# Optimization experiments

Measured on AMD Instinct MI355X. Metric: run time of the kernel, lower is better.

The kernel has to match this reference:

```python
import jax, jax.numpy as jnp
import numpy as np

D2 = 200  # 2*D with D=100, hidden size of H and U

def setup_inputs() -> dict:
    key = jax.random.key(0)
    k1, k2, k3, k4 = jax.random.split(key, 4)
    B, T, J = 64, 2048, 128
    H = jax.random.normal(k1, (B, T, D2), dtype=jnp.float32)
    U = jax.random.normal(k2, (B, J, D2), dtype=jnp.float32)
    # alpha = nn.Linear(6D, 1): weight [600], bias scalar
    bound = 1.0 / np.sqrt(6 * 100)
    w = jax.random.uniform(k3, (3 * D2,), minval=-bound, maxval=bound, dtype=jnp.float32)
    b = jax.random.uniform(k4, (), minval=-bound, maxval=bound, dtype=jnp.float32)
    return {"H": H, "U": U, "w": w, "b": b}

def reference(H, U, w, b):
    # Trilinear similarity S[b,t,j] = alpha([H_t; U_j; H_t*U_j]) decomposed:
    # identical math to concat+linear, without materializing [B,T*J,6D].
    w_h, w_u, w_m = w[:D2], w[D2:2 * D2], w[2 * D2:]
    S = (jnp.einsum('btd,d->bt', H, w_h)[:, :, None]
         + jnp.einsum('bjd,d->bj', U, w_u)[:, None, :]
         + jnp.einsum('btd,d,bjd->btj', H, w_m, U)
         + b)  # [B,T,J]
    C2Q_att = jax.nn.softmax(S, axis=-1)            # [B,T,J]
    U_tilde = jnp.einsum('btj,bjd->btd', C2Q_att, U)  # [B,T,2D]
    Q2C_att = jax.nn.softmax(jnp.max(S, axis=-1), axis=-1)  # [B,T]
    H_tilde = jnp.einsum('bt,btd->bd', Q2C_att, H)[:, None, :]  # [B,1,2D]
    T = H.shape[1]
    H_tilde_rep = jnp.broadcast_to(H_tilde, H.shape)  # repeat(1,T,1)
    G = jnp.concatenate([H, U_tilde, H * U_tilde, H * H_tilde_rep], axis=-1)  # [B,T,8D]
    return G, Q2C_att[:, None, :]
```

## Files before the change

### kernel.cpp

```cpp
#include <hip/hip_runtime.h>
#include <math.h>

typedef __attribute__((ext_vector_type(8))) short bf16x8;
typedef __attribute__((ext_vector_type(4))) float f32x4;

#define Bb 64
#define Tt 2048
#define Jj 128
#define Dd 200
#define GD 800
#define TILE 64
#define NTH 1024

#define OFF_USH 0u
#define OFF_UJT 57344u
#define OFF_HMS 110592u
#define OFF_PSH 139264u
#define OFF_SUS 155648u
#define OFF_SHS 156160u
#define OFF_SMX 156416u
#define OFF_SSM 157440u
#define SMEM_BYTES 158464u

__device__ __forceinline__ unsigned short f2bf(float f) {
    union { float f; unsigned u; } v; v.f = f;
    unsigned r = v.u + 0x7FFFu + ((v.u >> 16) & 1u);
    return (unsigned short)(r >> 16);
}

__device__ __forceinline__ bf16x8 pack8(f32x4 a, f32x4 b) {
    bf16x8 o;
    o[0] = (short)f2bf(a[0]); o[1] = (short)f2bf(a[1]);
    o[2] = (short)f2bf(a[2]); o[3] = (short)f2bf(a[3]);
    o[4] = (short)f2bf(b[0]); o[5] = (short)f2bf(b[1]);
    o[6] = (short)f2bf(b[2]); o[7] = (short)f2bf(b[3]);
    return o;
}

__global__ __launch_bounds__(NTH) void k_main(
    const float* __restrict__ H, const float* __restrict__ U,
    const float* __restrict__ wt, const float* __restrict__ bptr,
    float* __restrict__ G, float* __restrict__ mrow)
{
    __shared__ __align__(16) char smem[SMEM_BYTES];

    const int tid  = threadIdx.x;
    const int lane = tid & 63;
    const int wv   = tid >> 6;

    const int lin = blockIdx.x;
    const int wg  = (lin & 7) * 256 + (lin >> 3);
    const int b   = wg >> 5;
    const int t0  = (wg & 31) * TILE;

    const float* Hb = H + ((size_t)b * Tt + t0) * Dd;
    const float* Ub = U + (size_t)b * Jj * Dd;
    const float  bb = bptr[0];

    const float wh0 = wt[lane], wh1 = wt[64 + lane], wh2 = wt[128 + lane];
    const float wh3 = (lane < 8) ? wt[192 + lane] : 0.f;
    const float wu0 = wt[200 + lane], wu1 = wt[264 + lane], wu2 = wt[328 + lane];
    const float wu3 = (lane < 8) ? wt[392 + lane] : 0.f;

    for (int i = tid; i < 128 * 28; i += NTH) {
        int row = i / 28, c8 = i % 28;
        bf16x8 val = {0,0,0,0,0,0,0,0};
        if (c8 < 25) {
            const float* p = Ub + row * Dd + c8 * 8;
            val = pack8(*(const f32x4*)p, *(const f32x4*)(p + 4));
        }
        unsigned a = OFF_USH + (unsigned)row * 448u + (unsigned)c8 * 16u;
        *(bf16x8*)(smem + (a ^ ((unsigned)(row & 7) << 4))) = val;
    }
    for (int i = tid; i < TILE * 28; i += NTH) {
        int row = i / 28, c8 = i % 28;
        bf16x8 val = {0,0,0,0,0,0,0,0};
        if (c8 < 25) {
            const float* p  = Hb + row * Dd + c8 * 8;
            const float* wp = wt + 400 + c8 * 8;
            f32x4 h0 = *(const f32x4*)p,        h1 = *(const f32x4*)(p + 4);
            f32x4 w0 = *(const f32x4*)wp,       w1 = *(const f32x4*)(wp + 4);
            val = pack8(h0 * w0, h1 * w1);
        }
        unsigned a = OFF_HMS + (unsigned)row * 448u + (unsigned)c8 * 16u;
        *(bf16x8*)(smem + (a ^ ((unsigned)(row & 7) << 4))) = val;
    }
    for (int jj = 0; jj < 8; ++jj) {
        int j = wv * 8 + jj;
        const float* up = Ub + j * Dd;
        float v = up[lane] * wu0 + up[64 + lane] * wu1 + up[128 + lane] * wu2;
        if (lane < 8) v += up[192 + lane] * wu3;
        #pragma unroll
        for (int off = 32; off; off >>= 1) v += __shfl_xor(v, off);
        if (lane == 0) *(float*)(smem + OFF_SUS + (unsigned)j * 4u) = v + bb;
    }
    for (int rr = 0; rr < 4; ++rr) {
        int row = wv * 4 + rr;
        const float* hp = Hb + row * Dd;
        float v = hp[lane] * wh0 + hp[64 + lane] * wh1 + hp[128 + lane] * wh2;
        if (lane < 8) v += hp[192 + lane] * wh3;
        #pragma unroll
        for (int off = 32; off; off >>= 1) v += __shfl_xor(v, off);
        if (lane == 0) *(float*)(smem + OFF_SHS + (unsigned)row * 4u) = v;
    }
    __syncthreads();

    for (int i = tid; i < 208 * 64; i += NTH) {
        int d  = i >> 6;
        int jp = (i & 63) << 1;
        unsigned short v0 = 0, v1 = 0;
        if (d < Dd) {
            unsigned a0 = OFF_USH + (unsigned)jp * 448u + ((unsigned)d << 1);
            v0 = *(const unsigned short*)(smem + (a0 ^ ((unsigned)(jp & 7) << 4)));
            unsigned a1 = OFF_USH + (unsigned)(jp + 1) * 448u + ((unsigned)d << 1);
            v1 = *(const unsigned short*)(smem + (a1 ^ ((unsigned)((jp + 1) & 7) << 4)));
        }
        unsigned pk = (unsigned)v0 | ((unsigned)v1 << 16);
        unsigned wa = OFF_UJT + (unsigned)d * 256u + (unsigned)((i & 63) << 2);
        *(unsigned*)(smem + (wa ^ ((unsigned)(d & 7) << 4))) = pk;
    }

    const int rg = wv >> 2, cgS = wv & 3;
    const int rowA = rg * 16 + (lane & 15);
    const unsigned kfo = (unsigned)(((lane >> 4) << 4));
    f32x4 accS0 = {0.f, 0.f, 0.f, 0.f}, accS1 = {0.f, 0.f, 0.f, 0.f};
    #pragma unroll
    for (int ki = 0; ki < 7; ++ki) {
        unsigned ab = OFF_HMS + (unsigned)rowA * 448u + (unsigned)ki * 64u + kfo;
        bf16x8 af = *(const bf16x8*)(smem + (ab ^ ((unsigned)(rowA & 7) << 4)));
        int j0 = cgS * 32 + (lane & 15);
        unsigned b0 = OFF_USH + (unsigned)j0 * 448u + (unsigned)ki * 64u + kfo;
        bf16x8 bf0 = *(const bf16x8*)(smem + (b0 ^ ((unsigned)(j0 & 7) << 4)));
        accS0 = __builtin_amdgcn_mfma_f32_16x16x32_bf16(af, bf0, accS0, 0, 0, 0);
        int j1 = j0 + 16;
        unsigned b1 = OFF_USH + (unsigned)j1 * 448u + (unsigned)ki * 64u + kfo;
        bf16x8 bf1 = *(const bf16x8*)(smem + (b1 ^ ((unsigned)(j1 & 7) << 4)));
        accS1 = __builtin_amdgcn_mfma_f32_16x16x32_bf16(af, bf1, accS1, 0, 0, 0);
    }
    __syncthreads();

    const int rowBase = rg * 16 + ((lane >> 4) << 2);
    const float su0 = *(const float*)(smem + OFF_SUS + (unsigned)(cgS * 32 + (lane & 15)) * 4u);
    const float su1 = *(const float*)(smem + OFF_SUS + (unsigned)(cgS * 32 + 16 + (lane & 15)) * 4u);
    f32x4 sh4 = *(const f32x4*)(smem + OFF_SHS + (unsigned)rowBase * 4u);
    float s0a[4], s1a[4], e0a[4], e1a[4];
    #pragma unroll
    for (int r = 0; r < 4; ++r) {
        float s0 = accS0[r] + sh4[r] + su0;
        float s1 = accS1[r] + sh4[r] + su1;
        s0a[r] = s0; s1a[r] = s1;
        float m = fmaxf(s0, s1);
        m = fmaxf(m, __shfl_xor(m, 1));
        m = fmaxf(m, __shfl_xor(m, 2));
        m = fmaxf(m, __shfl_xor(m, 4));
        m = fmaxf(m, __shfl_xor(m, 8));
        if ((lane & 15) == 0)
            *(float*)(smem + OFF_SMX + (unsigned)((rowBase + r) * 4 + cgS) * 4u) = m;
    }
    __syncthreads();
    #pragma unroll
    for (int r = 0; r < 4; ++r) {
        f32x4 mx4 = *(const f32x4*)(smem + OFF_SMX + (unsigned)(rowBase + r) * 16u);
        float M = fmaxf(fmaxf(mx4[0], mx4[1]), fmaxf(mx4[2], mx4[3]));
        float e0 = __expf(s0a[r] - M), e1 = __expf(s1a[r] - M);
        e0a[r] = e0; e1a[r] = e1;
        float s = e0 + e1;
        s += __shfl_xor(s, 1); s += __shfl_xor(s, 2);
        s += __shfl_xor(s, 4); s += __shfl_xor(s, 8);
        if ((lane & 15) == 0)
            *(float*)(smem + OFF_SSM + (unsigned)((rowBase + r) * 4 + cgS) * 4u) = s;
        if (cgS == 0 && (lane & 15) == 0)
            mrow[(size_t)b * Tt + t0 + rowBase + r] = M;
    }
    __syncthreads();
    #pragma unroll
    for (int r = 0; r < 4; ++r) {
        f32x4 sm4 = *(const f32x4*)(smem + OFF_SSM + (unsigned)(rowBase + r) * 16u);
        float inv = 1.f / (sm4[0] + sm4[1] + sm4[2] + sm4[3]);
        float p0 = e0a[r] * inv, p1 = e1a[r] * inv;
        float pn0 = __shfl_down(p0, 1), pn1 = __shfl_down(p1, 1);
        if (!(lane & 1)) {
            int row = rowBase + r;
            int col0 = cgS * 32 + (lane & 15);
            unsigned swz = (unsigned)(row & 7) << 4;
            unsigned a0 = OFF_PSH + (unsigned)row * 256u + (unsigned)col0 * 2u;
            *(unsigned*)(smem + (a0 ^ swz)) = (unsigned)f2bf(p0) | ((unsigned)f2bf(pn0) << 16);
            unsigned a1 = a0 + 32u;
            *(unsigned*)(smem + (a1 ^ swz)) = (unsigned)f2bf(p1) | ((unsigned)f2bf(pn1) << 16);
        }
    }
    __syncthreads();

    const int rg2 = wv >> 2, cg2 = wv & 3;
    const int start = (cg2 == 0) ? 0 : (3 * cg2 + 1);
    const int cnt   = (cg2 == 0) ? 4 : 3;
    const int rowA2 = rg2 * 16 + (lane & 15);
    f32x4 accP0 = {0.f,0.f,0.f,0.f}, accP1 = {0.f,0.f,0.f,0.f};
    f32x4 accP2 = {0.f,0.f,0.f,0.f}, accP3 = {0.f,0.f,0.f,0.f};
    #pragma unroll
    for (int ki = 0; ki < 4; ++ki) {
        unsigned ab = OFF_PSH + (unsigned)rowA2 * 256u + (unsigned)ki * 64u + kfo;
        bf16x8 af = *(const bf16x8*)(smem + (ab ^ ((unsigned)(rowA2 & 7) << 4)));
        int d0 = start * 16 + (lane & 15);
        {
            unsigned bb0 = OFF_UJT + (unsigned)d0 * 256u + (unsigned)ki * 64u + kfo;
            bf16x8 bf = *(const bf16x8*)(smem + (bb0 ^ ((unsigned)(d0 & 7) << 4)));
            accP0 = __builtin_amdgcn_mfma_f32_16x16x32_bf16(af, bf, accP0, 0, 0, 0);
        }
        {
            int d = d0 + 16;
            unsigned bb1 = OFF_UJT + (unsigned)d * 256u + (unsigned)ki * 64u + kfo;
            bf16x8 bf = *(const bf16x8*)(smem + (bb1 ^ ((unsigned)(d & 7) << 4)));
            accP1 = __builtin_amdgcn_mfma_f32_16x16x32_bf16(af, bf, accP1, 0, 0, 0);
        }
        {
            int d = d0 + 32;
            unsigned bb2 = OFF_UJT + (unsigned)d * 256u + (unsigned)ki * 64u + kfo;
            bf16x8 bf = *(const bf16x8*)(smem + (bb2 ^ ((unsigned)(d & 7) << 4)));
            accP2 = __builtin_amdgcn_mfma_f32_16x16x32_bf16(af, bf, accP2, 0, 0, 0);
        }
        if (cnt == 4) {
            int d = d0 + 48;
            unsigned bb3 = OFF_UJT + (unsigned)d * 256u + (unsigned)ki * 64u + kfo;
            bf16x8 bf = *(const bf16x8*)(smem + (bb3 ^ ((unsigned)(d & 7) << 4)));
            accP3 = __builtin_amdgcn_mfma_f32_16x16x32_bf16(af, bf, accP3, 0, 0, 0);
        }
    }
    __syncthreads();

    {
        const int rowW = rg2 * 16 + ((lane >> 4) << 2);
        const int c0 = start * 16 + (lane & 15);
        #pragma unroll
        for (int r = 0; r < 4; ++r) {
            int row = rowW + r;
            float* base = (float*)(smem + OFF_UJT + (unsigned)row * 816u);
            base[c0]      = accP0[r];
            base[c0 + 16] = accP1[r];
            if (c0 + 32 < Dd) base[c0 + 32] = accP2[r];
            if (cnt == 4)     base[c0 + 48] = accP3[r];
        }
    }
    __syncthreads();

    for (int i = tid; i < TILE * 50; i += NTH) {
        int row = i / 50, c = i % 50;
        f32x4 ut = *(const f32x4*)(smem + OFF_UJT + (unsigned)row * 816u + (unsigned)c * 16u);
        f32x4 h4 = *(const f32x4*)(Hb + row * Dd + c * 4);
        float* grow = G + ((size_t)b * Tt + t0 + row) * GD + c * 4;
        *(f32x4*)(grow)       = h4;
        *(f32x4*)(grow + 200) = ut;
        *(f32x4*)(grow + 400) = h4 * ut;
    }
}

__global__ __launch_bounds__(256) void k_q(
    const float* __restrict__ mrow, float* __restrict__ q)
{
    __shared__ float red[4];
    __shared__ float sM, sS;
    const int b = blockIdx.x, tid = threadIdx.x;
    const int lane = tid & 63, wv = tid >> 6;
    const float* mb = mrow + (size_t)b * Tt;

    float lm = -1e30f;
    for (int i = tid; i < Tt; i += 256) lm = fmaxf(lm, mb[i]);
    #pragma unroll
    for (int off = 32; off; off >>= 1) lm = fmaxf(lm, __shfl_xor(lm, off));
    if (lane == 0) red[wv] = lm;
    __syncthreads();
    if (tid == 0) sM = fmaxf(fmaxf(red[0], red[1]), fmaxf(red[2], red[3]));
    __syncthreads();
    const float M = sM;

    float ls = 0.f;
    for (int i = tid; i < Tt; i += 256) ls += __expf(mb[i] - M);
    #pragma unroll
    for (int off = 32; off; off >>= 1) ls += __shfl_xor(ls, off);
    __syncthreads();
    if (lane == 0) red[wv] = ls;
    __syncthreads();
    if (tid == 0) sS = red[0] + red[1] + red[2] + red[3];
    __syncthreads();
    const float invS = 1.f / sS;

    for (int i = tid; i < Tt; i += 256)
        q[(size_t)b * Tt + i] = __expf(mb[i] - M) * invS;
}

__global__ __launch_bounds__(256) void k_ht(
    const float* __restrict__ H, const float* __restrict__ q,
    float* __restrict__ htil)
{
    const int b = blockIdx.y, ch = blockIdx.x;
    const int d4 = threadIdx.x & 63;
    const int tp = threadIdx.x >> 6;
    if (d4 >= 50) return;
    const float* Hb = H + (size_t)b * Tt * Dd;
    const float* qb = q + (size_t)b * Tt;
    f32x4 acc = {0.f, 0.f, 0.f, 0.f};
    const int tbase = ch * 128 + tp * 32;
    for (int k = 0; k < 32; ++k) {
        int t = tbase + k;
        f32x4 h4 = *(const f32x4*)(Hb + (size_t)t * Dd + d4 * 4);
        acc += h4 * qb[t];
    }
    float* hp = htil + b * Dd + d4 * 4;
    atomicAdd(hp + 0, acc[0]); atomicAdd(hp + 1, acc[1]);
    atomicAdd(hp + 2, acc[2]); atomicAdd(hp + 3, acc[3]);
}

__global__ __launch_bounds__(256) void k_g3(
    const float* __restrict__ H, const float* __restrict__ htil,
    float* __restrict__ G)
{
    const int idx = blockIdx.x * 256 + threadIdx.x;
    if (idx >= Bb * Tt * Dd) return;
    const int d  = idx % Dd;
    const int bt = idx / Dd;
    const int b  = bt >> 11;
    G[(size_t)bt * GD + 600 + d] = H[idx] * htil[b * Dd + d];
}

extern "C" void kernel_launch(void* const* d_in, const int* in_sizes, int n_in,
                              void* d_out, int out_size, void* d_ws, size_t ws_size,
                              hipStream_t stream)
{
    const float* H    = (const float*)d_in[0];
    const float* U    = (const float*)d_in[1];
    const float* wt   = (const float*)d_in[2];
    const float* bptr = (const float*)d_in[3];

    float* G    = (float*)d_out;
    float* q    = G + (size_t)Bb * Tt * GD;
    float* mrow = (float*)d_ws;
    float* htil = mrow + (size_t)Bb * Tt;

    hipMemsetAsync(htil, 0, (size_t)Bb * Dd * sizeof(float), stream);

    k_main<<<(Tt / TILE) * Bb, NTH, 0, stream>>>(H, U, wt, bptr, G, mrow);

    k_q<<<Bb, 256, 0, stream>>>(mrow, q);

    dim3 g2(Tt / 128, Bb);
    k_ht<<<g2, 256, 0, stream>>>(H, q, htil);

    const int n3 = Bb * Tt * Dd;
    k_g3<<<(n3 + 255) / 256, 256, 0, stream>>>(H, htil, G);
}
```

Measured before the change: 712.3 us.

## Make main kernel persistent over 16 tiles with double-buffered H staging

```diff
diff --git a/kernel.cpp b/kernel.cpp
--- a/kernel.cpp
+++ b/kernel.cpp
@@ -9,18 +9,20 @@
 #define Jj 128
 #define Dd 200
 #define GD 800
-#define TILE 64
+#define TILE 32
+#define NT 16
+#define ROWS_BLK (TILE*NT)
 #define NTH 1024
 
 #define OFF_USH 0u
 #define OFF_UJT 57344u
 #define OFF_HMS 110592u
 #define OFF_PSH 139264u
-#define OFF_SUS 155648u
-#define OFF_SHS 156160u
-#define OFF_SMX 156416u
-#define OFF_SSM 157440u
-#define SMEM_BYTES 158464u
+#define OFF_SUS 147456u
+#define OFF_SHS 147968u
+#define OFF_SMX 148224u
+#define OFF_SSM 149248u
+#define SMEM_BYTES 150272u
 
 __device__ __forceinline__ unsigned short f2bf(float f) {
     union { float f; unsigned u; } v; v.f = f;
@@ -37,6 +39,30 @@
     return o;
 }
 
+__device__ __forceinline__ void stage_h(char* smem, const float* __restrict__ Hrows,
+                                        int tid, int buf,
+                                        f32x4 wmA, f32x4 wmB, f32x4 whA, f32x4 whB)
+{
+    const int row = tid >> 5, c = tid & 31;
+    float shp = 0.f;
+    bf16x8 val = {0,0,0,0,0,0,0,0};
+    if (c < 25) {
+        const float* p = Hrows + row * Dd + c * 8;
+        f32x4 h0 = *(const f32x4*)p, h1 = *(const f32x4*)(p + 4);
+        shp = h0[0]*whA[0] + h0[1]*whA[1] + h0[2]*whA[2] + h0[3]*whA[3]
+            + h1[0]*whB[0] + h1[1]*whB[1] + h1[2]*whB[2] + h1[3]*whB[3];
+        val = pack8(h0 * wmA, h1 * wmB);
+    }
+    if (c < 28) {
+        unsigned a = OFF_HMS + (unsigned)buf * 14336u + (unsigned)row * 448u + (unsigned)c * 16u;
+        *(bf16x8*)(smem + (a ^ ((unsigned)(row & 7) << 4))) = val;
+    }
+    #pragma unroll
+    for (int off = 16; off; off >>= 1) shp += __shfl_xor(shp, off);
+    if ((tid & 31) == 0)
+        *(float*)(smem + OFF_SHS + (unsigned)buf * 128u + (unsigned)row * 4u) = shp;
+}
+
 __global__ __launch_bounds__(NTH) void k_main(
     const float* __restrict__ H, const float* __restrict__ U,
     const float* __restrict__ wt, const float* __restrict__ bptr,
@@ -48,17 +74,20 @@
     const int lane = tid & 63;
     const int wv   = tid >> 6;
 
-    const int lin = blockIdx.x;
-    const int wg  = (lin & 7) * 256 + (lin >> 3);
-    const int b   = wg >> 5;
-    const int t0  = (wg & 31) * TILE;
+    const int swz = ((blockIdx.x & 7) << 5) | (blockIdx.x >> 3);
+    const int b   = swz >> 2;
+    const int t0  = (swz & 3) * ROWS_BLK;
 
     const float* Hb = H + ((size_t)b * Tt + t0) * Dd;
     const float* Ub = U + (size_t)b * Jj * Dd;
     const float  bb = bptr[0];
 
-    const float wh0 = wt[lane], wh1 = wt[64 + lane], wh2 = wt[128 + lane];
-    const float wh3 = (lane < 8) ? wt[192 + lane] : 0.f;
+    const int cc = tid & 31;
+    f32x4 whA = {0,0,0,0}, whB = {0,0,0,0}, wmA = {0,0,0,0}, wmB = {0,0,0,0};
+    if (cc < 25) {
+        whA = *(const f32x4*)(wt + cc * 8);       whB = *(const f32x4*)(wt + cc * 8 + 4);
+        wmA = *(const f32x4*)(wt + 400 + cc * 8); wmB = *(const f32x4*)(wt + 400 + cc * 8 + 4);
+    }
     const float wu0 = wt[200 + lane], wu1 = wt[264 + lane], wu2 = wt[328 + lane];
     const float wu3 = (lane < 8) ? wt[392 + lane] : 0.f;
 
@@ -72,19 +101,7 @@
         unsigned a = OFF_USH + (unsigned)row * 448u + (unsigned)c8 * 16u;
         *(bf16x8*)(smem + (a ^ ((unsigned)(row & 7) << 4))) = val;
     }
-    for (int i = tid; i < TILE * 28; i += NTH) {
-        int row = i / 28, c8 = i % 28;
-        bf16x8 val = {0,0,0,0,0,0,0,0};
-        if (c8 < 25) {
-            const float* p  = Hb + row * Dd + c8 * 8;
-            const float* wp = wt + 400 + c8 * 8;
-            f32x4 h0 = *(const f32x4*)p,        h1 = *(const f32x4*)(p + 4);
-            f32x4 w0 = *(const f32x4*)wp,       w1 = *(const f32x4*)(wp + 4);
-            val = pack8(h0 * w0, h1 * w1);
-        }
-        unsigned a = OFF_HMS + (unsigned)row * 448u + (unsigned)c8 * 16u;
-        *(bf16x8*)(smem + (a ^ ((unsigned)(row & 7) << 4))) = val;
-    }
+    stage_h(smem, Hb, tid, 0, wmA, wmB, whA, whB);
     for (int jj = 0; jj < 8; ++jj) {
         int j = wv * 8 + jj;
         const float* up = Ub + j * Dd;
@@ -93,15 +110,6 @@
         #pragma unroll
         for (int off = 32; off; off >>= 1) v += __shfl_xor(v, off);
         if (lane == 0) *(float*)(smem + OFF_SUS + (unsigned)j * 4u) = v + bb;
-    }
-    for (int rr = 0; rr < 4; ++rr) {
-        int row = wv * 4 + rr;
-        const float* hp = Hb + row * Dd;
-        float v = hp[lane] * wh0 + hp[64 + lane] * wh1 + hp[128 + lane] * wh2;
-        if (lane < 8) v += hp[192 + lane] * wh3;
-        #pragma unroll
-        for (int off = 32; off; off >>= 1) v += __shfl_xor(v, off);
-        if (lane == 0) *(float*)(smem + OFF_SHS + (unsigned)row * 4u) = v;
     }
     __syncthreads();
 
@@ -120,137 +128,131 @@
         *(unsigned*)(smem + (wa ^ ((unsigned)(d & 7) << 4))) = pk;
     }
 
-    const int rg = wv >> 2, cgS = wv & 3;
-    const int rowA = rg * 16 + (lane & 15);
-    const unsigned kfo = (unsigned)(((lane >> 4) << 4));
-    f32x4 accS0 = {0.f, 0.f, 0.f, 0.f}, accS1 = {0.f, 0.f, 0.f, 0.f};
-    #pragma unroll
-    for (int ki = 0; ki < 7; ++ki) {
-        unsigned ab = OFF_HMS + (unsigned)rowA * 448u + (unsigned)ki * 64u + kfo;
-        bf16x8 af = *(const bf16x8*)(smem + (ab ^ ((unsigned)(rowA & 7) << 4)));
-        int j0 = cgS * 32 + (lane & 15);
-        unsigned b0 = OFF_USH + (unsigned)j0 * 448u + (unsigned)ki * 64u + kfo;
-        bf16x8 bf0 = *(const bf16x8*)(smem + (b0 ^ ((unsigned)(j0 & 7) << 4)));
-        accS0 = __builtin_amdgcn_mfma_f32_16x16x32_bf16(af, bf0, accS0, 0, 0, 0);
-        int j1 = j0 + 16;
-        unsigned b1 = OFF_USH + (unsigned)j1 * 448u + (unsigned)ki * 64u + kfo;
-        bf16x8 bf1 = *(const bf16x8*)(smem + (b1 ^ ((unsigned)(j1 & 7) << 4)));
-        accS1 = __builtin_amdgcn_mfma_f32_16x16x32_bf16(af, bf1, accS1, 0, 0, 0);
-    }
-    __syncthreads();
-
-    const int rowBase = rg * 16 + ((lane >> 4) << 2);
-    const float su0 = *(const float*)(smem + OFF_SUS + (unsigned)(cgS * 32 + (lane & 15)) * 4u);
-    const float su1 = *(const float*)(smem + OFF_SUS + (unsigned)(cgS * 32 + 16 + (lane & 15)) * 4u);
-    f32x4 sh4 = *(const f32x4*)(smem + OFF_SHS + (unsigned)rowBase * 4u);
-    float s0a[4], s1a[4], e0a[4], e1a[4];
-    #pragma unroll
-    for (int r = 0; r < 4; ++r) {
-        float s0 = accS0[r] + sh4[r] + su0;
-        float s1 = accS1[r] + sh4[r] + su1;
-        s0a[r] = s0; s1a[r] = s1;
-        float m = fmaxf(s0, s1);
-        m = fmaxf(m, __shfl_xor(m, 1));
-        m = fmaxf(m, __shfl_xor(m, 2));
-        m = fmaxf(m, __shfl_xor(m, 4));
-        m = fmaxf(m, __shfl_xor(m, 8));
-        if ((lane & 15) == 0)
-            *(float*)(smem + OFF_SMX + (unsigned)((rowBase + r) * 4 + cgS) * 4u) = m;
-    }
-    __syncthreads();
-    #pragma unroll
-    for (int r = 0; r < 4; ++r) {
-        f32x4 mx4 = *(const f32x4*)(smem + OFF_SMX + (unsigned)(rowBase + r) * 16u);
-        float M = fmaxf(fmaxf(mx4[0], mx4[1]), fmaxf(mx4[2], mx4[3]));
-        float e0 = __expf(s0a[r] - M), e1 = __expf(s1a[r] - M);
-        e0a[r] = e0; e1a[r] = e1;
-        float s = e0 + e1;
-        s += __shfl_xor(s, 1); s += __shfl_xor(s, 2);
-        s += __shfl_xor(s, 4); s += __shfl_xor(s, 8);
-        if ((lane & 15) == 0)
-            *(float*)(smem + OFF_SSM + (unsigned)((rowBase + r) * 4 + cgS) * 4u) = s;
-        if (cgS == 0 && (lane & 15) == 0)
-            mrow[(size_t)b * Tt + t0 + rowBase + r] = M;
-    }
-    __syncthreads();
-    #pragma unroll
-    for (int r = 0; r < 4; ++r) {
-        f32x4 sm4 = *(const f32x4*)(smem + OFF_SSM + (unsigned)(rowBase + r) * 16u);
-        float inv = 1.f / (sm4[0] + sm4[1] + sm4[2] + sm4[3]);
-        float p0 = e0a[r] * inv, p1 = e1a[r] * inv;
-        float pn0 = __shfl_down(p0, 1), pn1 = __shfl_down(p1, 1);
-        if (!(lane & 1)) {
+    const int rg  = wv >> 3;
+    const int cg  = wv & 7;
+    const int l15 = lane & 15;
+    const int lq  = lane >> 4;
+    const unsigned kfo = (unsigned)(lq << 4);
+    const int rowA    = rg * 16 + l15;
+    const int rowBase = rg * 16 + (lq << 2);
+    const int jcol    = cg * 16 + l15;
+    const int  dt0  = cg, dt1 = cg + 8;
+    const bool has2 = (dt1 < 13);
+    const int  dcol0 = dt0 * 16 + l15;
+    const int  dcol1 = dt1 * 16 + l15;
+
+    const unsigned hswz = (unsigned)(rowA & 7) << 4;
+    const unsigned ubase = OFF_USH + (unsigned)jcol * 448u;
+    const unsigned uswz  = (unsigned)(jcol & 7) << 4;
+    const unsigned pbase = OFF_PSH + (unsigned)rowA * 256u;
+    const unsigned pswz  = (unsigned)(rowA & 7) << 4;
+
+    for (int tile = 0; tile < NT; ++tile) {
+        const int cur = tile & 1, nxt = cur ^ 1;
+        const float* Ht = Hb + (size_t)tile * TILE * Dd;
+
+        if (tile + 1 < NT)
+            stage_h(smem, Ht + TILE * Dd, tid, nxt, wmA, wmB, whA, whB);
+
+        f32x4 acc = {0.f, 0.f, 0.f, 0.f};
+        const unsigned hbase = OFF_HMS + (unsigned)cur * 14336u + (unsigned)rowA * 448u;
+        #pragma unroll
+        for (int ki = 0; ki < 7; ++ki) {
+            bf16x8 af = *(const bf16x8*)(smem + ((hbase + (unsigned)ki * 64u + kfo) ^ hswz));
+            bf16x8 bf = *(const bf16x8*)(smem + ((ubase + (unsigned)ki * 64u + kfo) ^ uswz));
+            acc = __builtin_amdgcn_mfma_f32_16x16x32_bf16(af, bf, acc, 0, 0, 0);
+        }
+
+        const float suv = *(const float*)(smem + OFF_SUS + (unsigned)jcol * 4u);
+        f32x4 sh4 = *(const f32x4*)(smem + OFF_SHS + (unsigned)cur * 128u + (unsigned)rowBase * 4u);
+        float sv[4], ev[4], Mv[4];
+        #pragma unroll
+        for (int r = 0; r < 4; ++r) {
+            float s = acc[r] + sh4[r] + suv;
+            sv[r] = s;
+            float m = s;
+            m = fmaxf(m, __shfl_xor(m, 1));
+            m = fmaxf(m, __shfl_xor(m, 2));
+            m = fmaxf(m, __shfl_xor(m, 4));
+            m = fmaxf(m, __shfl_xor(m, 8));
+            if (l15 == 0)
+                *(float*)(smem + OFF_SMX + (unsigned)((rowBase + r) * 8 + cg) * 4u) = m;
+        }
+        __syncthreads();
+        #pragma unroll
+        for (int r = 0; r < 4; ++r) {
+            f32x4 ma = *(const f32x4*)(smem + OFF_SMX + (unsigned)(rowBase + r) * 32u);
+            f32x4 mb2 = *(const f32x4*)(smem + OFF_SMX + (unsigned)(rowBase + r) * 32u + 16u);
+            float M = fmaxf(fmaxf(fmaxf(ma[0], ma[1]), fmaxf(ma[2], ma[3])),
+                            fmaxf(fmaxf(mb2[0], mb2[1]), fmaxf(mb2[2], mb2[3])));
+            Mv[r] = M;
+            float e = __expf(sv[r] - M);
+            ev[r] = e;
+            float ssum = e;
+            ssum += __shfl_xor(ssum, 1); ssum += __shfl_xor(ssum, 2);
+            ssum += __shfl_xor(ssum, 4); ssum += __shfl_xor(ssum, 8);
+            if (l15 == 0)
+                *(float*)(smem + OFF_SSM + (unsigned)((rowBase + r) * 8 + cg) * 4u) = ssum;
+        }
+        if (cg == 0 && l15 == 0) {
+            #pragma unroll
+            for (int r = 0; r < 4; ++r)
+                mrow[(size_t)b * Tt + t0 + tile * TILE + rowBase + r] = Mv[r];
+        }
+        __syncthreads();
+        #pragma unroll
+        for (int r = 0; r < 4; ++r) {
+            f32x4 sa = *(const f32x4*)(smem + OFF_SSM + (unsigned)(rowBase + r) * 32u);
+            f32x4 sb = *(const f32x4*)(smem + OFF_SSM + (unsigned)(rowBase + r) * 32u + 16u);
+            float inv = 1.f / (sa[0] + sa[1] + sa[2] + sa[3] + sb[0] + sb[1] + sb[2] + sb[3]);
+            float p  = ev[r] * inv;
+            float pn = __shfl_down(p, 1);
+            if (!(lane & 1)) {
+                int row = rowBase + r;
+                unsigned a0 = OFF_PSH + (unsigned)row * 256u + (unsigned)jcol * 2u;
+                *(unsigned*)(smem + (a0 ^ ((unsigned)(row & 7) << 4))) =
+                    (unsigned)f2bf(p) | ((unsigned)f2bf(pn) << 16);
+            }
+        }
+        __syncthreads();
+
+        f32x4 acc0 = {0.f,0.f,0.f,0.f}, acc1 = {0.f,0.f,0.f,0.f};
+        #pragma unroll
+        for (int ki = 0; ki < 4; ++ki) {
+            bf16x8 af = *(const bf16x8*)(smem + ((pbase + (unsigned)ki * 64u + kfo) ^ pswz));
+            bf16x8 b0 = *(const bf16x8*)(smem +
+                ((OFF_UJT + (unsigned)dcol0 * 256u + (unsigned)ki * 64u + kfo) ^ ((unsigned)(dcol0 & 7) << 4)));
+            acc0 = __builtin_amdgcn_mfma_f32_16x16x32_bf16(af, b0, acc0, 0, 0, 0);
+            if (has2) {
+                bf16x8 b1 = *(const bf16x8*)(smem +
+                    ((OFF_UJT + (unsigned)dcol1 * 256u + (unsigned)ki * 64u + kfo) ^ ((unsigned)(dcol1 & 7) << 4)));
+                acc1 = __builtin_amdgcn_mfma_f32_16x16x32_bf16(af, b1, acc1, 0, 0, 0);
+            }
+        }
+
+        float* Gtile = G + ((size_t)b * Tt + t0 + tile * TILE) * GD;
+        #pragma unroll
+        for (int r = 0; r < 4; ++r) {
             int row = rowBase + r;
-            int col0 = cgS * 32 + (lane & 15);
-            unsigned swz = (unsigned)(row & 7) << 4;
-            unsigned a0 = OFF_PSH + (unsigned)row * 256u + (unsigned)col0 * 2u;
-            *(unsigned*)(smem + (a0 ^ swz)) = (unsigned)f2bf(p0) | ((unsigned)f2bf(pn0) << 16);
-            unsigned a1 = a0 + 32u;
-            *(unsigned*)(smem + (a1 ^ swz)) = (unsigned)f2bf(p1) | ((unsigned)f2bf(pn1) << 16);
-        }
-    }
-    __syncthreads();
-
-    const int rg2 = wv >> 2, cg2 = wv & 3;
-    const int start = (cg2 == 0) ? 0 : (3 * cg2 + 1);
-    const int cnt   = (cg2 == 0) ? 4 : 3;
-    const int rowA2 = rg2 * 16 + (lane & 15);
-    f32x4 accP0 = {0.f,0.f,0.f,0.f}, accP1 = {0.f,0.f,0.f,0.f};
-    f32x4 accP2 = {0.f,0.f,0.f,0.f}, accP3 = {0.f,0.f,0.f,0.f};
-    #pragma unroll
-    for (int ki = 0; ki < 4; ++ki) {
-        unsigned ab = OFF_PSH + (unsigned)rowA2 * 256u + (unsigned)ki * 64u + kfo;
-        bf16x8 af = *(const bf16x8*)(smem + (ab ^ ((unsigned)(rowA2 & 7) << 4)));
-        int d0 = start * 16 + (lane & 15);
-        {
-            unsigned bb0 = OFF_UJT + (unsigned)d0 * 256u + (unsigned)ki * 64u + kfo;
-            bf16x8 bf = *(const bf16x8*)(smem + (bb0 ^ ((unsigned)(d0 & 7) << 4)));
-            accP0 = __builtin_amdgcn_mfma_f32_16x16x32_bf16(af, bf, accP0, 0, 0, 0);
-        }
-        {
-            int d = d0 + 16;
-            unsigned bb1 = OFF_UJT + (unsigned)d * 256u + (unsigned)ki * 64u + kfo;
-            bf16x8 bf = *(const bf16x8*)(smem + (bb1 ^ ((unsigned)(d & 7) << 4)));
-            accP1 = __builtin_amdgcn_mfma_f32_16x16x32_bf16(af, bf, accP1, 0, 0, 0);
-        }
-        {
-            int d = d0 + 32;
-            unsigned bb2 = OFF_UJT + (unsigned)d * 256u + (unsigned)ki * 64u + kfo;
-            bf16x8 bf = *(const bf16x8*)(smem + (bb2 ^ ((unsigned)(d & 7) << 4)));
-            accP2 = __builtin_amdgcn_mfma_f32_16x16x32_bf16(af, bf, accP2, 0, 0, 0);
-        }
-        if (cnt == 4) {
-            int d = d0 + 48;
-            unsigned bb3 = OFF_UJT + (unsigned)d * 256u + (unsigned)ki * 64u + kfo;
-            bf16x8 bf = *(const bf16x8*)(smem + (bb3 ^ ((unsigned)(d & 7) << 4)));
-            accP3 = __builtin_amdgcn_mfma_f32_16x16x32_bf16(af, bf, accP3, 0, 0, 0);
-        }
-    }
-    __syncthreads();
-
-    {
-        const int rowW = rg2 * 16 + ((lane >> 4) << 2);
-        const int c0 = start * 16 + (lane & 15);
-        #pragma unroll
-        for (int r = 0; r < 4; ++r) {
-            int row = rowW + r;
-            float* base = (float*)(smem + OFF_UJT + (unsigned)row * 816u);
-            base[c0]      = accP0[r];
-            base[c0 + 16] = accP1[r];
-            if (c0 + 32 < Dd) base[c0 + 32] = accP2[r];
-            if (cnt == 4)     base[c0 + 48] = accP3[r];
-        }
-    }
-    __syncthreads();
-
-    for (int i = tid; i < TILE * 50; i += NTH) {
-        int row = i / 50, c = i % 50;
-        f32x4 ut = *(const f32x4*)(smem + OFF_UJT + (unsigned)row * 816u + (unsigned)c * 16u);
-        f32x4 h4 = *(const f32x4*)(Hb + row * Dd + c * 4);
-        float* grow = G + ((size_t)b * Tt + t0 + row) * GD + c * 4;
-        *(f32x4*)(grow)       = h4;
-        *(f32x4*)(grow + 200) = ut;
-        *(f32x4*)(grow + 400) = h4 * ut;
+            float* grow = Gtile + (size_t)row * GD;
+            {
+                float ut = acc0[r];
+                float h  = Ht[row * Dd + dcol0];
+                grow[200 + dcol0] = ut;
+                grow[400 + dcol0] = h * ut;
+            }
+            if (has2 && dcol1 < Dd) {
+                float ut = acc1[r];
+                float h  = Ht[row * Dd + dcol1];
+                grow[200 + dcol1] = ut;
+                grow[400 + dcol1] = h * ut;
+            }
+        }
+        for (int i = tid; i < TILE * 50; i += NTH) {
+            int row = i / 50, c = i % 50;
+            f32x4 h4 = *(const f32x4*)(Ht + row * Dd + c * 4);
+            *(f32x4*)(Gtile + (size_t)row * GD + c * 4) = h4;
+        }
     }
 }
 
@@ -315,11 +317,13 @@
     float* __restrict__ G)
 {
     const int idx = blockIdx.x * 256 + threadIdx.x;
-    if (idx >= Bb * Tt * Dd) return;
-    const int d  = idx % Dd;
-    const int bt = idx / Dd;
+    if (idx >= Bb * Tt * 50) return;
+    const int d4 = idx % 50;
+    const int bt = idx / 50;
     const int b  = bt >> 11;
-    G[(size_t)bt * GD + 600 + d] = H[idx] * htil[b * Dd + d];
+    f32x4 h4 = *(const f32x4*)(H + (size_t)bt * Dd + d4 * 4);
+    f32x4 t4 = *(const f32x4*)(htil + b * Dd + d4 * 4);
+    *(f32x4*)(G + (size_t)bt * GD + 600 + d4 * 4) = h4 * t4;
 }
 
 extern "C" void kernel_launch(void* const* d_in, const int* in_sizes, int n_in,
@@ -338,13 +342,13 @@
 
     hipMemsetAsync(htil, 0, (size_t)Bb * Dd * sizeof(float), stream);
 
-    k_main<<<(Tt / TILE) * Bb, NTH, 0, stream>>>(H, U, wt, bptr, G, mrow);
+    k_main<<<(Bb * Tt / ROWS_BLK), NTH, 0, stream>>>(H, U, wt, bptr, G, mrow);
 
     k_q<<<Bb, 256, 0, stream>>>(mrow, q);
 
     dim3 g2(Tt / 128, Bb);
     k_ht<<<g2, 256, 0, stream>>>(H, q, htil);
 
-    const int n3 = Bb * Tt * Dd;
+    const int n3 = Bb * Tt * 50;
     k_g3<<<(n3 + 255) / 256, 256, 0, stream>>>(H, htil, G);
 }
```

New measurement: 642.5 us. 1.11x faster.
